# Optimization experiments

Hardware: AMD Instinct MI355X
Metric: run time of the kernel (lower is better)

Reference implementation:

```python
import jax, jax.numpy as jnp
import numpy as np
from jax import lax

B = 32768
INPUT_SIZE = 42  # 1 rocket_y + 20*(rock_x, rock_y) + 1 speed
H, W = 10, 15    # grid_height, grid_width
OUT = 3


def setup_inputs() -> dict:
    key = jax.random.key(0)
    ks = jax.random.split(key, 8)
    p = lambda k, s: (jax.random.normal(k, s) * 0.05).astype(jnp.float32)
    x = (jax.random.uniform(ks[0], (B, INPUT_SIZE)) * 16.0).astype(jnp.float32)
    return {
        "x": x,
        "conv1_w": p(ks[1], (16, 2, 3, 3)), "conv1_b": jnp.zeros((16,), jnp.float32),
        "conv2_w": p(ks[2], (32, 16, 3, 3)), "conv2_b": jnp.zeros((32,), jnp.float32),
        "fc1_w": p(ks[3], (32 * H * W + 1, 256)), "fc1_b": jnp.zeros((256,), jnp.float32),
        "fc2_w": p(ks[4], (256, 128)), "fc2_b": jnp.zeros((128,), jnp.float32),
        "fc3_w": p(ks[5], (128, OUT)), "fc3_b": jnp.zeros((OUT,), jnp.float32),
    }


def _conv(h, w, b):
    # 3x3, stride 1, padding 1 (SAME), NCHW / OIHW
    return lax.conv_general_dilated(h, w, (1, 1), "SAME",
                                    dimension_numbers=("NCHW", "OIHW", "NCHW")) \
           + b[None, :, None, None]


def _build_grid(x):
    """Vectorized replacement of the per-sample Python scatter loop."""
    bsz = x.shape[0]
    b = jnp.arange(bsz)
    dt = x.dtype
    # rocket channel: grid[i, rocket_y, 1] = 1 if 0 <= rocket_y < H
    ry = x[:, 0].astype(jnp.int32)
    rv = ((ry >= 0) & (ry < H)).astype(dt)
    rocket = jnp.zeros((bsz, H, W), dt).at[b, jnp.clip(ry, 0, H - 1), 1].add(rv)
    # rock channel: pairs (x, y) at columns (1,2),(3,4),...,(39,40)
    kx = x[:, 1:INPUT_SIZE - 1:2].astype(jnp.int32)  # [B, 20]
    ky = x[:, 2:INPUT_SIZE - 1:2].astype(jnp.int32)  # [B, 20]
    kv = ((kx >= 0) & (ky >= 0) & (kx < W) & (ky < H)).astype(dt)
    rock = jnp.zeros((bsz, H, W), dt).at[
        b[:, None], jnp.clip(ky, 0, H - 1), jnp.clip(kx, 0, W - 1)
    ].max(kv)  # set-to-1 semantics (duplicates ok)
    return jnp.stack([rocket, rock], axis=1)  # [B, 2, H, W]


def reference(x, conv1_w, conv1_b, conv2_w, conv2_b,
              fc1_w, fc1_b, fc2_w, fc2_b, fc3_w, fc3_b):
    grid = _build_grid(x)
    h = jax.nn.relu(_conv(grid, conv1_w, conv1_b))
    h = jax.nn.relu(_conv(h, conv2_w, conv2_b))
    h = h.reshape(x.shape[0], -1)                      # NCHW flatten, matches torch .view
    h = jnp.concatenate([h, x[:, -1:]], axis=1)        # append speed
    h = jax.nn.relu(h @ fc1_w + fc1_b)
    h = jax.nn.relu(h @ fc2_w + fc2_b)
    return h @ fc3_w + fc3_b
```

## Files before the change

kernel.cpp:

```cpp
#include <hip/hip_runtime.h>
#include <hip/hip_bf16.h>
#include <stdint.h>

typedef short short8 __attribute__((ext_vector_type(8)));
typedef float f32x4  __attribute__((ext_vector_type(4)));

__device__ __forceinline__ uint16_t f2bf(float f) {
    union { float f; uint32_t u; } v; v.f = f;
    return (uint16_t)((v.u + 0x7FFFu + ((v.u >> 16) & 1u)) >> 16);
}
__device__ __forceinline__ float bf2f(uint16_t h) {
    union { uint32_t u; float f; } v; v.u = ((uint32_t)h) << 16;
    return v.f;
}
__device__ __forceinline__ uint32_t pk2bf(float a, float b) {
    uint32_t r;
    asm("v_cvt_pk_bf16_f32 %0, %1, %2" : "=v"(r) : "v"(a), "v"(b));
    return r;
}
__device__ __forceinline__ void gl_lds16(const void* g, void* l) {
    __builtin_amdgcn_global_load_lds(
        (const __attribute__((address_space(1))) unsigned int*)g,
        (__attribute__((address_space(3))) unsigned int*)l, 16, 0, 0);
}

#define NSAMP_TOT 32768
#define H2_PER_S  5120

__global__ void repack_all(const float* __restrict__ f1w, const float* __restrict__ c2w,
                           const float* __restrict__ c1w, const float* __restrict__ f2w,
                           uint16_t* __restrict__ w1pt, uint16_t* __restrict__ w2rt,
                           uint16_t* __restrict__ w1rt, uint16_t* __restrict__ w2bt) {
    int tid = threadIdx.x, b = blockIdx.x;
    if (b < 160) {
        int f_s = b >> 4, cp = b & 15, n = tid;
        __align__(16) uint16_t vals[32];
        #pragma unroll
        for (int o = 0; o < 32; o++) {
            int c = cp * 2 + (o >> 4), pl = o & 15;
            int p = f_s * 16 + pl;
            float v = (p < 150) ? f1w[(size_t)(c * 150 + p) * 256 + n] : 0.f;
            vals[o] = f2bf(v);
        }
        int win = f_s * 8 + (cp >> 1);
        size_t rowbase = (size_t)n * H2_PER_S + win * 64;
        #pragma unroll
        for (int j = 0; j < 4; j++) {
            int qlog = (cp * 4 + j) & 7;
            int qphy = qlog ^ (n & 7);
            *(uint4*)&w1pt[rowbase + qphy * 8] = *(uint4*)&vals[j * 8];
        }
    } else if (b == 160) {
        for (int t = tid; t < 32 * 160; t += 256) {
            int n = t / 160, k = t % 160;
            float v = 0.f;
            if (k < 144) {
                int tap = k >> 4, ci = k & 15, dy = tap / 3, dx = tap % 3;
                v = c2w[((n * 16 + ci) * 3 + dy) * 3 + dx];
            }
            w2rt[t] = f2bf(v);
        }
        for (int t = tid; t < 16 * 32; t += 256) {
            int n = t >> 5, k = t & 31;
            float v = 0.f;
            if (k < 18) {
                int tap = k >> 1, ch = k & 1;
                int dy = (tap * 11) >> 5, dx = tap - dy * 3;
                v = c1w[((n * 2 + ch) * 3 + dy) * 3 + dx];
            }
            w1rt[t] = f2bf(v);
        }
    } else {
        __shared__ float tr2[32][129];
        int kb = b - 161;
        for (int i = tid; i < 32 * 128; i += 256) {
            int kk = i >> 7, n = i & 127;
            tr2[kk][n] = f2w[(size_t)(kb * 32 + kk) * 128 + n];
        }
        __syncthreads();
        int n = tid >> 1, half = tid & 1;
        __align__(16) uint16_t tmp[16];
        #pragma unroll
        for (int q = 0; q < 16; q++) tmp[q] = f2bf(tr2[half * 16 + q][n]);
        *(uint4*)&w2bt[(size_t)n * 256 + kb * 32 + half * 16]     = *(uint4*)&tmp[0];
        *(uint4*)&w2bt[(size_t)n * 256 + kb * 32 + half * 16 + 8] = *(uint4*)&tmp[8];
    }
}

__launch_bounds__(512, 2)
__global__ void k12_fused(const float* __restrict__ x, const uint16_t* __restrict__ w1rt,
                          const float* __restrict__ c1b, const uint16_t* __restrict__ w2rt,
                          const float* __restrict__ c2b, uint16_t* __restrict__ h2, int s0) {
    __shared__ float sx[8 * 42];
    __shared__ __align__(16) uint16_t grd[8 * 204 * 2];
    __shared__ __align__(16) uint16_t h1s[8 * 205 * 16];
    __shared__ uint16_t lutPO[160];
    __shared__ uint16_t lutST[160];
    int tid = threadIdx.x;
    int w = tid >> 6, l = tid & 63, lr = l & 15, lk = l >> 4;

    short8 b1f = *(const short8*)&w1rt[lr * 32 + lk * 8];
    short8 bfr[5][2];
    #pragma unroll
    for (int ks = 0; ks < 5; ks++)
        #pragma unroll
        for (int nf = 0; nf < 2; nf++)
            bfr[ks][nf] = *(const short8*)&w2rt[(nf * 16 + lr) * 160 + ks * 32 + lk * 8];
    float cb1r = c1b[lr];
    float cb0 = c2b[lr], cb1 = c2b[16 + lr];

    uint4 z4 = make_uint4(0, 0, 0, 0);
    for (int idx = tid; idx < 3688; idx += 512) {
        if (idx < 408) ((uint4*)grd)[idx] = z4;
        else           ((uint4*)h1s)[idx - 408] = z4;
    }
    int sbase = s0 + blockIdx.x * 8;
    if (tid < 336) sx[tid] = x[(size_t)(sbase + tid / 42) * 42 + (tid % 42)];
    if (tid >= 336 && tid < 496) {
        int p = tid - 336;
        int y = p / 15, xx = p - y * 15;
        int po = y * 17 + xx;
        lutPO[p] = (p < 150) ? (uint16_t)po : 0;
        lutST[p] = (p < 150) ? (uint16_t)((po + 18) * 16) : (uint16_t)(204 * 16);
    }
    __syncthreads();

    if (tid < 160) {
        int sl = tid / 20, r = tid % 20;
        int kx = (int)sx[sl * 42 + 1 + 2 * r];
        int ky = (int)sx[sl * 42 + 2 + 2 * r];
        if (kx >= 0 && kx < 15 && ky >= 0 && ky < 10)
            grd[(sl * 204 + (ky + 1) * 17 + (kx + 1)) * 2 + 1] = 0x3F80;
    } else if (tid < 168) {
        int sl = tid - 160;
        int ry = (int)sx[sl * 42];
        if (ry >= 0 && ry < 10)
            grd[(sl * 204 + (ry + 1) * 17 + 2) * 2 + 0] = 0x3F80;
    }
    __syncthreads();

    int goff[4]; uint32_t gmask[4];
    #pragma unroll
    for (int jj = 0; jj < 4; jj++) {
        int t = lk * 4 + jj;
        int tc = t < 9 ? t : 0;
        int dy = (tc * 11) >> 5, dx = tc - dy * 3;
        goff[jj] = dy * 17 + dx;
        gmask[jj] = (t < 9) ? 0xFFFFFFFFu : 0u;
    }
    int sbg  = w * 204;
    int sb16 = w * 205 * 16;

    #pragma unroll
    for (int f_s = 0; f_s < 10; f_s++) {
        int p160 = f_s * 16 + lr;
        int gbase = sbg + lutPO[p160];
        union { uint32_t d[4]; short8 s; } au;
        #pragma unroll
        for (int jj = 0; jj < 4; jj++) {
            uint32_t v = *(const uint32_t*)&grd[(gbase + goff[jj]) * 2];
            au.d[jj] = v & gmask[jj];
        }
        f32x4 acc = {};
        acc = __builtin_amdgcn_mfma_f32_16x16x32_bf16(au.s, b1f, acc, 0, 0, 0);
        #pragma unroll
        for (int j = 0; j < 4; j += 2) {
            float v0 = fmaxf(acc[j] + cb1r, 0.f);
            float v1 = fmaxf(acc[j + 1] + cb1r, 0.f);
            uint32_t pk = pk2bf(v0, v1);
            int p2 = f_s * 16 + lk * 4 + j;
            h1s[sb16 + lutST[p2] + lr]     = (uint16_t)pk;
            h1s[sb16 + lutST[p2 + 1] + lr] = (uint16_t)(pk >> 16);
        }
    }
    __syncthreads();

    int cdofs[5];
    #pragma unroll
    for (int ks = 0; ks < 5; ks++) {
        int idx = ks * 4 + lk;
        int idc = idx < 18 ? idx : 0;
        int tap = idc >> 1, half = idc & 1;
        int dy = (tap * 11) >> 5, dx = tap - dy * 3;
        cdofs[ks] = (dy * 17 + dx) * 16 + half * 8;
    }
    uint32_t kmask4 = ((16 + lk) < 18) ? 0xFFFFFFFFu : 0u;
    int k0lo = lr * 16 + lk * 4;
    int k0s_base = (k0lo & ~63) | ((((k0lo >> 3) & 7) ^ w) << 3) | (k0lo & 7);
    size_t sbh2 = (size_t)(blockIdx.x * 8 + w) * H2_PER_S;

    #pragma unroll
    for (int f_s = 0; f_s < 10; f_s++) {
        int p160 = f_s * 16 + lr;
        int abase = sb16 + lutPO[p160] * 16;
        f32x4 acc0 = {}, acc1 = {};
        #pragma unroll
        for (int ks = 0; ks < 5; ks++) {
            short8 av = *(const short8*)&h1s[abase + cdofs[ks]];
            if (ks == 4) {
                union { short8 s; uint32_t d[4]; } u; u.s = av;
                #pragma unroll
                for (int dd = 0; dd < 4; dd++) u.d[dd] &= kmask4;
                av = u.s;
            }
            acc0 = __builtin_amdgcn_mfma_f32_16x16x32_bf16(av, bfr[ks][0], acc0, 0, 0, 0);
            acc1 = __builtin_amdgcn_mfma_f32_16x16x32_bf16(av, bfr[ks][1], acc1, 0, 0, 0);
        }
        uint32_t p01 = pk2bf(fmaxf(acc0[0] + cb0, 0.f), fmaxf(acc0[1] + cb0, 0.f));
        uint32_t p23 = pk2bf(fmaxf(acc0[2] + cb0, 0.f), fmaxf(acc0[3] + cb0, 0.f));
        uint32_t q01 = pk2bf(fmaxf(acc1[0] + cb1, 0.f), fmaxf(acc1[1] + cb1, 0.f));
        uint32_t q23 = pk2bf(fmaxf(acc1[2] + cb1, 0.f), fmaxf(acc1[3] + cb1, 0.f));
        int k0s = f_s * 512 + k0s_base;
        *(uint2*)&h2[sbh2 + k0s]       = make_uint2(p01, p23);
        *(uint2*)&h2[sbh2 + k0s + 256] = make_uint2(q01, q23);
    }
}

__launch_bounds__(512)
__global__ void k3_fused(const uint16_t* __restrict__ h2, const uint16_t* __restrict__ w1pt,
                         const float* __restrict__ f1b, const float* __restrict__ f1w,
                         const float* __restrict__ x, const uint16_t* __restrict__ w2bt,
                         const float* __restrict__ f2b, const float* __restrict__ f3w,
                         const float* __restrict__ f3b, float* __restrict__ out, int s0) {
    #define BUF_E (64 * 64 + 256 * 64)
    __shared__ __align__(16) uint16_t uLDS[3 * BUF_E];
    uint16_t* lH = uLDS;
    __shared__ float sbias[256], swl[256], sspeed[64], sb2[128], sw3[384];
    __shared__ float pf[4][64][3];
    int tid = threadIdx.x;
    int bm = blockIdx.x;
    if (tid < 256) { sbias[tid] = f1b[tid]; swl[tid] = f1w[(size_t)4800 * 256 + tid]; }
    else if (tid < 320) sspeed[tid - 256] = x[(size_t)(s0 + bm * 64 + (tid - 256)) * 42 + 41];
    else if (tid < 448) sb2[tid - 320] = f2b[tid - 320];
    for (int i = tid; i < 384; i += 512) sw3[i] = f3w[i];

    int w = tid >> 6, l = tid & 63, lr = l & 15, lk = l >> 4;
    int wm = w >> 2, wn = w & 3;
    const uint16_t* ga = &h2[(size_t)(bm * 64 + (tid >> 3)) * H2_PER_S + (tid & 7) * 8];
    const uint16_t* gb[4];
    #pragma unroll
    for (int i = 0; i < 4; i++) {
        int c2 = tid + i * 512;
        gb[i] = &w1pt[(size_t)(c2 >> 3) * H2_PER_S + (c2 & 7) * 8];
    }
    int saOff = tid * 8;
    int sbOff[4];
    #pragma unroll
    for (int i = 0; i < 4; i++) sbOff[i] = 4096 + (tid + i * 512) * 8;
    int aoff[2][2], boff[4][2];
    #pragma unroll
    for (int ks = 0; ks < 2; ks++) {
        int cl = (ks * 4 + lk);
        #pragma unroll
        for (int mf = 0; mf < 2; mf++)
            aoff[mf][ks] = (wm * 32 + mf * 16 + lr) * 64 + ((cl ^ (lr & 7)) << 3);
        #pragma unroll
        for (int nf = 0; nf < 4; nf++)
            boff[nf][ks] = 4096 + (wn * 64 + nf * 16 + lr) * 64 + ((cl ^ (lr & 7)) << 3);
    }

    uint16_t* bufA = uLDS;
    uint16_t* bufB = uLDS + BUF_E;
    uint16_t* bufC = uLDS + 2 * BUF_E;

    f32x4 acc[2][4] = {};
    gl_lds16(ga, bufA + saOff); ga += 64;
    #pragma unroll
    for (int i = 0; i < 4; i++) { gl_lds16(gb[i], bufA + sbOff[i]); gb[i] += 64; }
    gl_lds16(ga, bufB + saOff); ga += 64;
    #pragma unroll
    for (int i = 0; i < 4; i++) { gl_lds16(gb[i], bufB + sbOff[i]); gb[i] += 64; }

    for (int kt = 0; kt < 80; kt++) {
        if (kt < 79) asm volatile("s_waitcnt vmcnt(5)" ::: "memory");
        else         asm volatile("s_waitcnt vmcnt(0)" ::: "memory");
        __builtin_amdgcn_s_barrier();
        __builtin_amdgcn_sched_barrier(0);
        if (kt < 78) {
            gl_lds16(ga, bufC + saOff); ga += 64;
            #pragma unroll
            for (int i = 0; i < 4; i++) { gl_lds16(gb[i], bufC + sbOff[i]); gb[i] += 64; }
        }
        #pragma unroll
        for (int ks = 0; ks < 2; ks++) {
            short8 a[2], b[4];
            #pragma unroll
            for (int mf = 0; mf < 2; mf++)
                a[mf] = *(const short8*)&bufA[aoff[mf][ks]];
            #pragma unroll
            for (int nf = 0; nf < 4; nf++)
                b[nf] = *(const short8*)&bufA[boff[nf][ks]];
            #pragma unroll
            for (int mf = 0; mf < 2; mf++)
                #pragma unroll
                for (int nf = 0; nf < 4; nf++)
                    acc[mf][nf] = __builtin_amdgcn_mfma_f32_16x16x32_bf16(a[mf], b[nf], acc[mf][nf], 0, 0, 0);
        }
        uint16_t* t = bufA; bufA = bufB; bufB = bufC; bufC = t;
    }
    __syncthreads();
    #pragma unroll
    for (int mf = 0; mf < 2; mf++) {
        #pragma unroll
        for (int j = 0; j < 4; j++) {
            int r = wm * 32 + mf * 16 + lk * 4 + j;
            float sp = sspeed[r];
            #pragma unroll
            for (int nf = 0; nf < 4; nf++) {
                int col = wn * 64 + nf * 16 + lr;
                float v = acc[mf][nf][j] + sbias[col] + sp * swl[col];
                int cc = col >> 3, cl = col & 7;
                lH[r * 256 + ((cc ^ (r & 7)) << 3) + cl] = f2bf(v > 0.f ? v : 0.f);
            }
        }
    }
    __syncthreads();
    f32x4 acc2[2][2] = {};
    #pragma unroll
    for (int ks2 = 0; ks2 < 8; ks2++) {
        short8 a2[2], bv[2];
        #pragma unroll
        for (int mf2 = 0; mf2 < 2; mf2++) {
            int row = wm * 32 + mf2 * 16 + lr;
            int chunk = (ks2 * 4 + lk) ^ (row & 7);
            a2[mf2] = *(const short8*)&lH[row * 256 + chunk * 8];
        }
        #pragma unroll
        for (int nf2 = 0; nf2 < 2; nf2++)
            bv[nf2] = *(const short8*)&w2bt[(size_t)(wn * 32 + nf2 * 16 + lr) * 256 + ks2 * 32 + lk * 8];
        #pragma unroll
        for (int mf2 = 0; mf2 < 2; mf2++)
            #pragma unroll
            for (int nf2 = 0; nf2 < 2; nf2++)
                acc2[mf2][nf2] = __builtin_amdgcn_mfma_f32_16x16x32_bf16(a2[mf2], bv[nf2], acc2[mf2][nf2], 0, 0, 0);
    }
    float p3[2][4][3];
    #pragma unroll
    for (int mf2 = 0; mf2 < 2; mf2++)
        #pragma unroll
        for (int j = 0; j < 4; j++)
            #pragma unroll
            for (int o = 0; o < 3; o++) p3[mf2][j][o] = 0.f;
    #pragma unroll
    for (int mf2 = 0; mf2 < 2; mf2++) {
        #pragma unroll
        for (int nf2 = 0; nf2 < 2; nf2++) {
            int col = wn * 32 + nf2 * 16 + lr;
            float w0 = sw3[col * 3 + 0], w1v = sw3[col * 3 + 1], w2v = sw3[col * 3 + 2];
            #pragma unroll
            for (int j = 0; j < 4; j++) {
                float v = acc2[mf2][nf2][j] + sb2[col];
                v = v > 0.f ? v : 0.f;
                p3[mf2][j][0] += v * w0;
                p3[mf2][j][1] += v * w1v;
                p3[mf2][j][2] += v * w2v;
            }
        }
    }
    #pragma unroll
    for (int off = 1; off < 16; off <<= 1)
        #pragma unroll
        for (int mf2 = 0; mf2 < 2; mf2++)
            #pragma unroll
            for (int j = 0; j < 4; j++)
                #pragma unroll
                for (int o = 0; o < 3; o++)
                    p3[mf2][j][o] += __shfl_xor(p3[mf2][j][o], off);
    if (lr == 0) {
        #pragma unroll
        for (int mf2 = 0; mf2 < 2; mf2++)
            #pragma unroll
            for (int j = 0; j < 4; j++) {
                int r = wm * 32 + mf2 * 16 + lk * 4 + j;
                #pragma unroll
                for (int o = 0; o < 3; o++) pf[wn][r][o] = p3[mf2][j][o];
            }
    }
    __syncthreads();
    if (tid < 192) {
        int r = tid / 3, o = tid - r * 3;
        out[(size_t)(s0 + bm * 64 + r) * 3 + o] =
            pf[0][r][o] + pf[1][r][o] + pf[2][r][o] + pf[3][r][o] + f3b[o];
    }
    #undef BUF_E
}

extern "C" void kernel_launch(void* const* d_in, const int* in_sizes, int n_in,
                              void* d_out, int out_size, void* d_ws, size_t ws_size,
                              hipStream_t stream) {
    const float* x   = (const float*)d_in[0];
    const float* c1w = (const float*)d_in[1];
    const float* c1b = (const float*)d_in[2];
    const float* c2w = (const float*)d_in[3];
    const float* c2b = (const float*)d_in[4];
    const float* f1w = (const float*)d_in[5];
    const float* f1b = (const float*)d_in[6];
    const float* f2w = (const float*)d_in[7];
    const float* f2b = (const float*)d_in[8];
    const float* f3w = (const float*)d_in[9];
    const float* f3b = (const float*)d_in[10];
    float* out = (float*)d_out;

    char* ws = (char*)d_ws;
    uint16_t* w1pt = (uint16_t*)ws;
    uint16_t* w2rt = (uint16_t*)(ws + 2621440);
    uint16_t* w2bt = (uint16_t*)(ws + 2631680);
    uint16_t* w1rt = (uint16_t*)(ws + 2697216);
    size_t base = 2698240;

    int chunk = NSAMP_TOT;
    while (chunk > 128 && base + (size_t)chunk * 10240 > ws_size) chunk >>= 1;
    uint16_t* h2 = (uint16_t*)(ws + base);

    repack_all<<<169, 256, 0, stream>>>(f1w, c2w, c1w, f2w, w1pt, w2rt, w1rt, w2bt);

    for (int s0 = 0; s0 < NSAMP_TOT; s0 += chunk) {
        k12_fused<<<chunk / 8, 512, 0, stream>>>(x, w1rt, c1b, w2rt, c2b, h2, s0);
        k3_fused<<<chunk / 64, 512, 0, stream>>>(h2, w1pt, f1b, f1w, x, w2bt, f2b, f3w, f3b, out, s0);
    }
}
```

Measured before the change: 266.6 us.

## Double fc1 GEMM M-tile to 128 rows with two-stage double buffering

The fused fc1/fc2/fc3 kernel now handles 128 samples per block instead of 64. Each wave computes 64x64 of the fc1 output, so every loaded slice of the fc1 weight is reused across twice as many rows, which halves weight traffic per sample. The three-buffer pipeline with explicit vmcnt waits is replaced by a simpler two-buffer scheme that uses a full __syncthreads each k-step. That adds synchronisation, gives less load/compute overlap, doubles the accumulator registers (possible occupancy loss), and halves the grid size.

```diff
diff --git a/kernel.cpp b/kernel.cpp
--- a/kernel.cpp
+++ b/kernel.cpp
@@ -222,88 +222,82 @@
                          const float* __restrict__ x, const uint16_t* __restrict__ w2bt,
                          const float* __restrict__ f2b, const float* __restrict__ f3w,
                          const float* __restrict__ f3b, float* __restrict__ out, int s0) {
-    #define BUF_E (64 * 64 + 256 * 64)
-    __shared__ __align__(16) uint16_t uLDS[3 * BUF_E];
+    #define BUF_E (128 * 64 + 256 * 64)
+    __shared__ __align__(16) uint16_t uLDS[2 * BUF_E];
     uint16_t* lH = uLDS;
-    __shared__ float sbias[256], swl[256], sspeed[64], sb2[128], sw3[384];
-    __shared__ float pf[4][64][3];
+    __shared__ float sbias[256], swl[256], sspeed[128], sb2[128], sw3[384];
+    __shared__ float pf[4][128][3];
     int tid = threadIdx.x;
     int bm = blockIdx.x;
-    if (tid < 256) { sbias[tid] = f1b[tid]; swl[tid] = f1w[(size_t)4800 * 256 + tid]; }
-    else if (tid < 320) sspeed[tid - 256] = x[(size_t)(s0 + bm * 64 + (tid - 256)) * 42 + 41];
-    else if (tid < 448) sb2[tid - 320] = f2b[tid - 320];
+    if (tid < 256)      { sbias[tid] = f1b[tid]; swl[tid] = f1w[(size_t)4800 * 256 + tid]; }
+    else if (tid < 384) sspeed[tid - 256] = x[(size_t)(s0 + bm * 128 + (tid - 256)) * 42 + 41];
+    else                sb2[tid - 384] = f2b[tid - 384];
     for (int i = tid; i < 384; i += 512) sw3[i] = f3w[i];
 
     int w = tid >> 6, l = tid & 63, lr = l & 15, lk = l >> 4;
     int wm = w >> 2, wn = w & 3;
-    const uint16_t* ga = &h2[(size_t)(bm * 64 + (tid >> 3)) * H2_PER_S + (tid & 7) * 8];
+    const uint16_t* ga0 = &h2[(size_t)(bm * 128 + (tid >> 3)) * H2_PER_S + (tid & 7) * 8];
+    const uint16_t* ga1 = &h2[(size_t)(bm * 128 + 64 + (tid >> 3)) * H2_PER_S + (tid & 7) * 8];
     const uint16_t* gb[4];
     #pragma unroll
     for (int i = 0; i < 4; i++) {
         int c2 = tid + i * 512;
         gb[i] = &w1pt[(size_t)(c2 >> 3) * H2_PER_S + (c2 & 7) * 8];
     }
-    int saOff = tid * 8;
+    int saOff0 = tid * 8, saOff1 = 4096 + tid * 8;
     int sbOff[4];
     #pragma unroll
-    for (int i = 0; i < 4; i++) sbOff[i] = 4096 + (tid + i * 512) * 8;
-    int aoff[2][2], boff[4][2];
+    for (int i = 0; i < 4; i++) sbOff[i] = 8192 + (tid + i * 512) * 8;
+    int aoff[4][2], boff[4][2];
     #pragma unroll
     for (int ks = 0; ks < 2; ks++) {
         int cl = (ks * 4 + lk);
         #pragma unroll
-        for (int mf = 0; mf < 2; mf++)
-            aoff[mf][ks] = (wm * 32 + mf * 16 + lr) * 64 + ((cl ^ (lr & 7)) << 3);
+        for (int mf = 0; mf < 4; mf++)
+            aoff[mf][ks] = (wm * 64 + mf * 16 + lr) * 64 + ((cl ^ (lr & 7)) << 3);
         #pragma unroll
         for (int nf = 0; nf < 4; nf++)
-            boff[nf][ks] = 4096 + (wn * 64 + nf * 16 + lr) * 64 + ((cl ^ (lr & 7)) << 3);
-    }
-
-    uint16_t* bufA = uLDS;
-    uint16_t* bufB = uLDS + BUF_E;
-    uint16_t* bufC = uLDS + 2 * BUF_E;
-
-    f32x4 acc[2][4] = {};
-    gl_lds16(ga, bufA + saOff); ga += 64;
-    #pragma unroll
-    for (int i = 0; i < 4; i++) { gl_lds16(gb[i], bufA + sbOff[i]); gb[i] += 64; }
-    gl_lds16(ga, bufB + saOff); ga += 64;
-    #pragma unroll
-    for (int i = 0; i < 4; i++) { gl_lds16(gb[i], bufB + sbOff[i]); gb[i] += 64; }
-
+            boff[nf][ks] = 8192 + (wn * 64 + nf * 16 + lr) * 64 + ((cl ^ (lr & 7)) << 3);
+    }
+
+    f32x4 acc[4][4] = {};
+    gl_lds16(ga0, uLDS + saOff0); ga0 += 64;
+    gl_lds16(ga1, uLDS + saOff1); ga1 += 64;
+    #pragma unroll
+    for (int i = 0; i < 4; i++) { gl_lds16(gb[i], uLDS + sbOff[i]); gb[i] += 64; }
+    __syncthreads();
     for (int kt = 0; kt < 80; kt++) {
-        if (kt < 79) asm volatile("s_waitcnt vmcnt(5)" ::: "memory");
-        else         asm volatile("s_waitcnt vmcnt(0)" ::: "memory");
-        __builtin_amdgcn_s_barrier();
-        __builtin_amdgcn_sched_barrier(0);
-        if (kt < 78) {
-            gl_lds16(ga, bufC + saOff); ga += 64;
-            #pragma unroll
-            for (int i = 0; i < 4; i++) { gl_lds16(gb[i], bufC + sbOff[i]); gb[i] += 64; }
-        }
+        int cur = kt & 1;
+        uint16_t* nbuf = uLDS + (cur ^ 1) * BUF_E;
+        if (kt < 79) {
+            gl_lds16(ga0, nbuf + saOff0); ga0 += 64;
+            gl_lds16(ga1, nbuf + saOff1); ga1 += 64;
+            #pragma unroll
+            for (int i = 0; i < 4; i++) { gl_lds16(gb[i], nbuf + sbOff[i]); gb[i] += 64; }
+        }
+        const uint16_t* buf = uLDS + cur * BUF_E;
         #pragma unroll
         for (int ks = 0; ks < 2; ks++) {
-            short8 a[2], b[4];
-            #pragma unroll
-            for (int mf = 0; mf < 2; mf++)
-                a[mf] = *(const short8*)&bufA[aoff[mf][ks]];
+            short8 a[4], b[4];
+            #pragma unroll
+            for (int mf = 0; mf < 4; mf++)
+                a[mf] = *(const short8*)&buf[aoff[mf][ks]];
             #pragma unroll
             for (int nf = 0; nf < 4; nf++)
-                b[nf] = *(const short8*)&bufA[boff[nf][ks]];
-            #pragma unroll
-            for (int mf = 0; mf < 2; mf++)
+                b[nf] = *(const short8*)&buf[boff[nf][ks]];
+            #pragma unroll
+            for (int mf = 0; mf < 4; mf++)
                 #pragma unroll
                 for (int nf = 0; nf < 4; nf++)
                     acc[mf][nf] = __builtin_amdgcn_mfma_f32_16x16x32_bf16(a[mf], b[nf], acc[mf][nf], 0, 0, 0);
         }
-        uint16_t* t = bufA; bufA = bufB; bufB = bufC; bufC = t;
-    }
-    __syncthreads();
-    #pragma unroll
-    for (int mf = 0; mf < 2; mf++) {
+        __syncthreads();
+    }
+    #pragma unroll
+    for (int mf = 0; mf < 4; mf++) {
         #pragma unroll
         for (int j = 0; j < 4; j++) {
-            int r = wm * 32 + mf * 16 + lk * 4 + j;
+            int r = wm * 64 + mf * 16 + lk * 4 + j;
             float sp = sspeed[r];
             #pragma unroll
             for (int nf = 0; nf < 4; nf++) {
@@ -315,13 +309,13 @@
         }
     }
     __syncthreads();
-    f32x4 acc2[2][2] = {};
+    f32x4 acc2[4][2] = {};
     #pragma unroll
     for (int ks2 = 0; ks2 < 8; ks2++) {
-        short8 a2[2], bv[2];
-        #pragma unroll
-        for (int mf2 = 0; mf2 < 2; mf2++) {
-            int row = wm * 32 + mf2 * 16 + lr;
+        short8 a2[4], bv[2];
+        #pragma unroll
+        for (int mf2 = 0; mf2 < 4; mf2++) {
+            int row = wm * 64 + mf2 * 16 + lr;
             int chunk = (ks2 * 4 + lk) ^ (row & 7);
             a2[mf2] = *(const short8*)&lH[row * 256 + chunk * 8];
         }
@@ -329,20 +323,20 @@
         for (int nf2 = 0; nf2 < 2; nf2++)
             bv[nf2] = *(const short8*)&w2bt[(size_t)(wn * 32 + nf2 * 16 + lr) * 256 + ks2 * 32 + lk * 8];
         #pragma unroll
-        for (int mf2 = 0; mf2 < 2; mf2++)
+        for (int mf2 = 0; mf2 < 4; mf2++)
             #pragma unroll
             for (int nf2 = 0; nf2 < 2; nf2++)
                 acc2[mf2][nf2] = __builtin_amdgcn_mfma_f32_16x16x32_bf16(a2[mf2], bv[nf2], acc2[mf2][nf2], 0, 0, 0);
     }
-    float p3[2][4][3];
-    #pragma unroll
-    for (int mf2 = 0; mf2 < 2; mf2++)
+    float p3[4][4][3];
+    #pragma unroll
+    for (int mf2 = 0; mf2 < 4; mf2++)
         #pragma unroll
         for (int j = 0; j < 4; j++)
             #pragma unroll
             for (int o = 0; o < 3; o++) p3[mf2][j][o] = 0.f;
     #pragma unroll
-    for (int mf2 = 0; mf2 < 2; mf2++) {
+    for (int mf2 = 0; mf2 < 4; mf2++) {
         #pragma unroll
         for (int nf2 = 0; nf2 < 2; nf2++) {
             int col = wn * 32 + nf2 * 16 + lr;
@@ -360,7 +354,7 @@
     #pragma unroll
     for (int off = 1; off < 16; off <<= 1)
         #pragma unroll
-        for (int mf2 = 0; mf2 < 2; mf2++)
+        for (int mf2 = 0; mf2 < 4; mf2++)
             #pragma unroll
             for (int j = 0; j < 4; j++)
                 #pragma unroll
@@ -368,18 +362,18 @@
                     p3[mf2][j][o] += __shfl_xor(p3[mf2][j][o], off);
     if (lr == 0) {
         #pragma unroll
-        for (int mf2 = 0; mf2 < 2; mf2++)
+        for (int mf2 = 0; mf2 < 4; mf2++)
             #pragma unroll
             for (int j = 0; j < 4; j++) {
-                int r = wm * 32 + mf2 * 16 + lk * 4 + j;
+                int r = wm * 64 + mf2 * 16 + lk * 4 + j;
                 #pragma unroll
                 for (int o = 0; o < 3; o++) pf[wn][r][o] = p3[mf2][j][o];
             }
     }
     __syncthreads();
-    if (tid < 192) {
+    if (tid < 384) {
         int r = tid / 3, o = tid - r * 3;
-        out[(size_t)(s0 + bm * 64 + r) * 3 + o] =
+        out[(size_t)(s0 + bm * 128 + r) * 3 + o] =
             pf[0][r][o] + pf[1][r][o] + pf[2][r][o] + pf[3][r][o] + f3b[o];
     }
     #undef BUF_E
@@ -416,6 +410,6 @@
 
     for (int s0 = 0; s0 < NSAMP_TOT; s0 += chunk) {
         k12_fused<<<chunk / 8, 512, 0, stream>>>(x, w1rt, c1b, w2rt, c2b, h2, s0);
-        k3_fused<<<chunk / 64, 512, 0, stream>>>(h2, w1pt, f1b, f1w, x, w2bt, f2b, f3w, f3b, out, s0);
-    }
-}
+        k3_fused<<<chunk / 128, 512, 0, stream>>>(h2, w1pt, f1b, f1w, x, w2bt, f2b, f3w, f3b, out, s0);
+    }
+}
```

After: 305.0 us. +14.4%, slower.
